# Kernel tuning notes

Hardware: AMD Instinct MI355X
Metric: run time of the kernel (lower is better)

The kernel has to match this reference:

```python
import jax, jax.numpy as jnp
import numpy as np

D_MODEL = 1024
N_HEADS = 16
D_K = D_MODEL // N_HEADS
SCALE = float(np.sqrt(D_K))


def setup_inputs() -> dict:
    key = jax.random.key(0)
    ks = jax.random.split(key, 6)
    B, S = 2, 2048
    lim_qkv = 1.0 / np.sqrt(D_MODEL)
    x = jax.random.normal(ks[0], (B, S, D_MODEL), dtype=jnp.float32)
    mask = jnp.ones((B, S), dtype=jnp.int32)
    W_qkv = jax.random.uniform(ks[1], (D_MODEL, 3 * D_MODEL), jnp.float32, -lim_qkv, lim_qkv)
    b_qkv = jax.random.uniform(ks[2], (3 * D_MODEL,), jnp.float32, -lim_qkv, lim_qkv)
    W_out = jax.random.uniform(ks[3], (D_MODEL, D_MODEL), jnp.float32, -lim_qkv, lim_qkv)
    b_out = jax.random.uniform(ks[4], (D_MODEL,), jnp.float32, -lim_qkv, lim_qkv)
    return {"x": x, "mask": mask, "W_qkv": W_qkv, "b_qkv": b_qkv, "W_out": W_out, "b_out": b_out}


def reference(x, mask, W_qkv, b_qkv, W_out, b_out):
    B, S, _ = x.shape
    qkv = x @ W_qkv + b_qkv                                  # [B,S,3*D]
    qkv = qkv.reshape(B, S, 3, N_HEADS, D_K)
    qkv = jnp.transpose(qkv, (2, 0, 3, 1, 4))                # [3,B,H,S,Dk]
    q, k, v = qkv[0], qkv[1], qkv[2]
    scores = jnp.einsum('bhqd,bhkd->bhqk', q, k) / SCALE      # [B,H,S,S]
    m = mask[:, None, None, :]                               # [B,1,1,S]
    scores = jnp.where(m == 0, jnp.float32(-1e9), scores)
    attn = jax.nn.softmax(scores, axis=-1)
    out = jnp.einsum('bhqk,bhkd->bhqd', attn, v)             # [B,H,S,Dk]
    out = jnp.transpose(out, (0, 2, 1, 3)).reshape(B, S, D_MODEL)
    return out @ W_out + b_out
```

## Files before the change

kernel.cpp:

```cpp
#include <hip/hip_runtime.h>
#include <hip/hip_bf16.h>

typedef __attribute__((ext_vector_type(8))) short short8;
typedef __attribute__((ext_vector_type(4))) short short4v;
typedef __attribute__((ext_vector_type(4))) float f32x4;
typedef __attribute__((ext_vector_type(16))) float f32x16;
typedef __attribute__((ext_vector_type(4))) unsigned uint4v;
typedef __attribute__((ext_vector_type(2))) unsigned uint2v;

static constexpr int BATCH = 2, S = 2048, D = 1024, H = 16, DK = 64;
static constexpr int TOK = BATCH * S;
static constexpr int NQKV = 3 * D;
static constexpr float C2 = 0.125f * 1.44269504088896f;

__device__ inline unsigned short f2bf(float f) {
  unsigned int u = __builtin_bit_cast(unsigned int, f);
  unsigned int r = (u + 0x7fffu + ((u >> 16) & 1u)) >> 16;
  return (unsigned short)r;
}

__device__ inline unsigned cvt_pk_bf16(float lo, float hi) {
  unsigned r;
  asm("v_cvt_pk_bf16_f32 %0, %1, %2" : "=v"(r) : "v"(lo), "v"(hi));
  return r;
}

__device__ inline uint2v permswap(unsigned a, unsigned b) {
  return __builtin_amdgcn_permlane32_swap(a, b, false, false);
}

__device__ inline float fexp2(float x) { return __builtin_amdgcn_exp2f(x); }

__device__ inline void gload_lds16(const void* g, void* l) {
  __builtin_amdgcn_global_load_lds((const __attribute__((address_space(1))) void*)g,
                                   (__attribute__((address_space(3))) void*)l, 16, 0, 0);
}

static constexpr int NB_CVT  = (TOK * D / 4) / 256;
static constexpr int NB_WQKV = (NQKV / 64) * (D / 64);
static constexpr int NB_WOUT = (D / 64) * (D / 64);
static constexpr int NB_MASK = TOK / 256;

__global__ __launch_bounds__(256) void k_prep(const float* __restrict__ x,
                                              unsigned short* __restrict__ x_bf,
                                              const float* __restrict__ W_qkv,
                                              unsigned short* __restrict__ wqkv_t,
                                              const float* __restrict__ W_out,
                                              unsigned short* __restrict__ wout_t,
                                              const int* __restrict__ mask,
                                              float* __restrict__ maskadd,
                                              unsigned char* __restrict__ tileflags) {
  __shared__ float tile[64][65];
  const int bi = blockIdx.x;
  const int tid = threadIdx.x;
  if (bi < NB_CVT) {
    const int i = bi * 256 + tid;
    const float4 v = ((const float4*)x)[i];
    short4v o;
    o[0] = (short)f2bf(v.x); o[1] = (short)f2bf(v.y);
    o[2] = (short)f2bf(v.z); o[3] = (short)f2bf(v.w);
    ((short4v*)x_bf)[i] = o;
    return;
  }
  if (bi < NB_CVT + NB_WQKV + NB_WOUT) {
    const int tbi = bi - NB_CVT;
    const float* in; unsigned short* out; int C, bx, by;
    if (tbi < NB_WQKV) { in = W_qkv; out = wqkv_t; C = NQKV; bx = tbi % (NQKV / 64); by = tbi / (NQKV / 64); }
    else { const int u = tbi - NB_WQKV; in = W_out; out = wout_t; C = D; bx = u % (D / 64); by = u / (D / 64); }
    const int bc = bx * 64, br = by * 64;
    const int lrow = tid >> 4, lc4 = (tid & 15) * 4;
#pragma unroll
    for (int p = 0; p < 4; ++p) {
      const float4 v = *(const float4*)(in + (size_t)(br + p * 16 + lrow) * C + bc + lc4);
      tile[p * 16 + lrow][lc4 + 0] = v.x;
      tile[p * 16 + lrow][lc4 + 1] = v.y;
      tile[p * 16 + lrow][lc4 + 2] = v.z;
      tile[p * 16 + lrow][lc4 + 3] = v.w;
    }
    __syncthreads();
    const int c = tid >> 2, seg = (tid & 3) * 16;
    uint4v w0, w1;
#pragma unroll
    for (int j = 0; j < 4; ++j) {
      w0[j] = cvt_pk_bf16(tile[seg + 2 * j][c], tile[seg + 2 * j + 1][c]);
      w1[j] = cvt_pk_bf16(tile[seg + 8 + 2 * j][c], tile[seg + 9 + 2 * j][c]);
    }
    unsigned short* dst = out + (size_t)(bc + c) * D + br + seg;
    *(uint4v*)dst = w0;
    *(uint4v*)(dst + 8) = w1;
    return;
  }
  {
    const int j = (bi - NB_CVT - NB_WQKV - NB_WOUT) * 256 + tid;
    const int mv = mask[j];
    maskadd[j] = mv ? 0.f : -1.0e9f;
    const unsigned long long bal = __ballot(mv == 0);
    if ((tid & 63) == 0) tileflags[j >> 6] = (bal != 0ull) ? 1 : 0;
  }
}

template <int QKV_MODE>
__global__ __launch_bounds__(256, 3) void k_gemm(const unsigned short* __restrict__ A,
                                                 const unsigned short* __restrict__ Bt,
                                                 const float* __restrict__ bias,
                                                 void* __restrict__ Cout,
                                                 unsigned short* __restrict__ vt,
                                                 int M, int N, int K) {
  __shared__ alignas(16) unsigned short As[128 * 64];
  __shared__ alignas(16) unsigned short Bs[128 * 64];
  const int tid = threadIdx.x;
  const int wid = tid >> 6, lane = tid & 63;
  const int lr = lane & 15, lg = lane >> 4;
  const int nbx = N >> 7;
  const int bx = blockIdx.x % nbx, by = blockIdx.x / nbx;
  const int m0 = by << 7, n0 = bx << 7;
  const int wm = (wid >> 1) << 6, wn = (wid & 1) << 6;

  f32x4 acc[4][4] = {};

  const int sk = ((lane & 7) ^ (lane >> 3)) << 4;
  const int srow = lane >> 3;

  const int ktc = K >> 6;
  for (int kt = 0; kt < ktc; ++kt) {
    const int k0 = kt << 6;
    __syncthreads();
#pragma unroll
    for (int c = 0; c < 4; ++c) {
      const int chunk = c * 4 + wid;
      const int mrow = chunk * 8 + srow;
      const char* ga = (const char*)(A + (size_t)(m0 + mrow) * K + k0) + sk;
      gload_lds16(ga, (char*)As + chunk * 1024);
      const char* gb = (const char*)(Bt + (size_t)(n0 + mrow) * K + k0) + sk;
      gload_lds16(gb, (char*)Bs + chunk * 1024);
    }
    __syncthreads();
#pragma unroll
    for (int ks = 0; ks < 2; ++ks) {
      const int kb = ks * 64 + lg * 16;
      const int swz = (lr & 7) << 4;
      short8 af[4], bfr[4];
#pragma unroll
      for (int mf = 0; mf < 4; ++mf) {
        const int m = wm + mf * 16 + lr;
        af[mf] = *(const short8*)((const char*)As + m * 128 + (kb ^ swz));
      }
#pragma unroll
      for (int nf = 0; nf < 4; ++nf) {
        const int n = wn + nf * 16 + lr;
        bfr[nf] = *(const short8*)((const char*)Bs + n * 128 + (kb ^ swz));
      }
#pragma unroll
      for (int mf = 0; mf < 4; ++mf)
#pragma unroll
        for (int nf = 0; nf < 4; ++nf)
          acc[mf][nf] = __builtin_amdgcn_mfma_f32_16x16x32_bf16(af[mf], bfr[nf], acc[mf][nf], 0, 0, 0);
    }
  }
#pragma unroll
  for (int nf = 0; nf < 4; ++nf) {
    const int n = n0 + wn + nf * 16 + lr;
    const float bv = bias[n];
    if (QKV_MODE) {
      if (n < 2 * D) {
        const float scl = (n < D) ? C2 : 1.0f;
#pragma unroll
        for (int mf = 0; mf < 4; ++mf)
#pragma unroll
          for (int r = 0; r < 4; ++r) {
            const int m = m0 + wm + mf * 16 + lg * 4 + r;
            ((unsigned short*)Cout)[(size_t)m * N + n] = f2bf((acc[mf][nf][r] + bv) * scl);
          }
      } else {
        const int dd = n - 2 * D;
        const int hh = dd >> 6, dk = dd & 63;
#pragma unroll
        for (int mf = 0; mf < 4; ++mf) {
          const int mbase = m0 + wm + mf * 16 + lg * 4;
          const int bb = mbase >> 11;
          const int ss = mbase & (S - 1);
          uint2 w;
          w.x = cvt_pk_bf16(acc[mf][nf][0] + bv, acc[mf][nf][1] + bv);
          w.y = cvt_pk_bf16(acc[mf][nf][2] + bv, acc[mf][nf][3] + bv);
          *(uint2*)(vt + ((size_t)((bb * H + hh) * DK + dk)) * S + ss) = w;
        }
      }
    } else {
#pragma unroll
      for (int mf = 0; mf < 4; ++mf)
#pragma unroll
        for (int r = 0; r < 4; ++r) {
          const int m = m0 + wm + mf * 16 + lg * 4 + r;
          ((float*)Cout)[(size_t)m * N + n] = acc[mf][nf][r] + bv;
        }
    }
  }
}

__global__ __launch_bounds__(256, 2) void k_attn(const unsigned short* __restrict__ qkv,
                                                 const unsigned short* __restrict__ vt,
                                                 const float* __restrict__ maskadd,
                                                 const unsigned char* __restrict__ tileflags,
                                                 unsigned short* __restrict__ attn) {
  __shared__ alignas(16) char Ks[2][16384];
  __shared__ alignas(16) char Vs[2][16384];

  constexpr int NT = S / 128;

  const int blk = blockIdx.x;
  const int work = (blk & 7) * 64 + (blk >> 3);
  const int qt = work & 15;
  const int bh = work >> 4;
  const int b = bh >> 4, h = bh & 15;
  const int tid = threadIdx.x;
  const int wid = tid >> 6, lane = tid & 63;
  const int l5 = lane & 31, hw = lane >> 5;
  const int q0 = qt * 128 + wid * 32;
  const int q = q0 + l5;

  const unsigned char* bflags = tileflags + b * (S / 64);

  const unsigned short* qrow = qkv + (size_t)(b * S + q) * NQKV + h * DK;
  short8 qf[4];
#pragma unroll
  for (int ks = 0; ks < 4; ++ks)
    qf[ks] = *(const short8*)(qrow + ks * 16 + hw * 8);

  const unsigned short* kg0 = qkv + ((size_t)b * S * NQKV + D + h * DK);
  const unsigned short* vg0 = vt + (size_t)bh * DK * S;
  const int srow8 = lane >> 3;
  const int skk = ((lane & 7) ^ srow8) << 4;
  const int vrow4 = lane >> 4;

  auto stage = [&](int buf, int kt) {
    const int kbase = kt * 128;
#pragma unroll
    for (int i = 0; i < 4; ++i) {
      const int ck = wid + i * 4;
      const int krow = ck * 8 + srow8;
      gload_lds16((const char*)(kg0 + (size_t)(kbase + krow) * NQKV) + skk,
                  Ks[buf] + ck * 1024);
      const int cv = wid + i * 4;
      const int vr = cv * 4 + vrow4;
      const int ss = (lane & 15) ^ (vr & 15);
      gload_lds16((const char*)(vg0 + (size_t)vr * S + kbase + ss * 8),
                  Vs[buf] + cv * 1024);
    }
  };

  f32x16 o[2] = {};
  float lpart = 0.f;

  const int rswz8 = (l5 & 7) << 4;
  const int rswz16 = (l5 & 15) << 4;

  stage(0, 0);

  int cur = 0;
  for (int kt = 0; kt < NT; ++kt) {
    asm volatile("s_waitcnt vmcnt(0)" ::: "memory");
    __builtin_amdgcn_s_barrier();
    __builtin_amdgcn_sched_barrier(0);
    if (kt + 1 < NT) stage(cur ^ 1, kt + 1);

    const int kbase = kt * 128;

    f32x16 sc[4];
    __builtin_amdgcn_s_setprio(1);
#pragma unroll
    for (int kh = 0; kh < 4; ++kh) {
      f32x16 t2 = {};
#pragma unroll
      for (int ks = 0; ks < 4; ++ks) {
        const short8 kf = *(const short8*)(Ks[cur] + (kh * 32 + l5) * 128 +
                                           ((ks * 32 + hw * 16) ^ rswz8));
        t2 = __builtin_amdgcn_mfma_f32_32x32x16_bf16(kf, qf[ks], t2, 0, 0, 0);
      }
      sc[kh] = t2;
    }
    __builtin_amdgcn_s_setprio(0);

    short8 vf[2][8];
#pragma unroll
    for (int dh = 0; dh < 2; ++dh)
#pragma unroll
      for (int s = 0; s < 8; ++s)
        vf[dh][s] = *(const short8*)(Vs[cur] + (dh * 32 + l5) * 256 +
                                     ((s * 32 + hw * 16) ^ rswz16));

    if (bflags[2 * kt] | bflags[2 * kt + 1]) {
#pragma unroll
      for (int kh = 0; kh < 4; ++kh)
#pragma unroll
        for (int m = 0; m < 4; ++m) {
          const f32x4 a4 = *(const f32x4*)(maskadd + b * S + kbase + kh * 32 + m * 8 + hw * 4);
#pragma unroll
          for (int r = 0; r < 4; ++r)
            sc[kh][m * 4 + r] += a4[r];
        }
    }

    float ps = 0.f;
#pragma unroll
    for (int kh = 0; kh < 4; ++kh) {
#pragma unroll
      for (int r = 0; r < 16; ++r)
        sc[kh][r] = fexp2(sc[kh][r]);
#pragma unroll
      for (int m = 0; m < 4; ++m)
        ps += (sc[kh][4 * m] + sc[kh][4 * m + 1]) + (sc[kh][4 * m + 2] + sc[kh][4 * m + 3]);

      const unsigned c00 = cvt_pk_bf16(sc[kh][0], sc[kh][1]);
      const unsigned c01 = cvt_pk_bf16(sc[kh][2], sc[kh][3]);
      const unsigned c10 = cvt_pk_bf16(sc[kh][4], sc[kh][5]);
      const unsigned c11 = cvt_pk_bf16(sc[kh][6], sc[kh][7]);
      const unsigned c20 = cvt_pk_bf16(sc[kh][8], sc[kh][9]);
      const unsigned c21 = cvt_pk_bf16(sc[kh][10], sc[kh][11]);
      const unsigned c30 = cvt_pk_bf16(sc[kh][12], sc[kh][13]);
      const unsigned c31 = cvt_pk_bf16(sc[kh][14], sc[kh][15]);
      const uint2v r0 = permswap(c00, c10);
      const uint2v r1 = permswap(c01, c11);
      const uint2v r2 = permswap(c20, c30);
      const uint2v r3 = permswap(c21, c31);
      uint4v p0, p1;
      p0[0] = r0[0]; p0[2] = r0[1]; p0[1] = r1[0]; p0[3] = r1[1];
      p1[0] = r2[0]; p1[2] = r2[1]; p1[1] = r3[0]; p1[3] = r3[1];
      const short8 pb0 = __builtin_bit_cast(short8, p0);
      const short8 pb1 = __builtin_bit_cast(short8, p1);

      __builtin_amdgcn_s_setprio(1);
#pragma unroll
      for (int dh = 0; dh < 2; ++dh) {
        o[dh] = __builtin_amdgcn_mfma_f32_32x32x16_bf16(vf[dh][2 * kh], pb0, o[dh], 0, 0, 0);
        o[dh] = __builtin_amdgcn_mfma_f32_32x32x16_bf16(vf[dh][2 * kh + 1], pb1, o[dh], 0, 0, 0);
      }
      __builtin_amdgcn_s_setprio(0);
    }
    lpart += ps;

    cur ^= 1;
  }

  const float ls = lpart + __shfl_xor(lpart, 32);
  const float inv = 1.0f / ls;
  unsigned short* orow = attn + (size_t)(b * S + q) * D + h * DK;
#pragma unroll
  for (int dh = 0; dh < 2; ++dh)
#pragma unroll
    for (int m = 0; m < 4; ++m) {
      const int d = dh * 32 + m * 8 + hw * 4;
      uint2 w;
      w.x = cvt_pk_bf16(o[dh][4 * m + 0] * inv, o[dh][4 * m + 1] * inv);
      w.y = cvt_pk_bf16(o[dh][4 * m + 2] * inv, o[dh][4 * m + 3] * inv);
      *(uint2*)(orow + d) = w;
    }
}

extern "C" void kernel_launch(void* const* d_in, const int* in_sizes, int n_in,
                              void* d_out, int out_size, void* d_ws, size_t ws_size,
                              hipStream_t stream) {
  const float* x = (const float*)d_in[0];
  const int* mask = (const int*)d_in[1];
  const float* W_qkv = (const float*)d_in[2];
  const float* b_qkv = (const float*)d_in[3];
  const float* W_out = (const float*)d_in[4];
  const float* b_out = (const float*)d_in[5];
  float* out = (float*)d_out;

  char* ws = (char*)d_ws;
  unsigned short* x_bf   = (unsigned short*)(ws);
  unsigned short* wqkv_t = (unsigned short*)(ws + (size_t)(8 << 20));
  unsigned short* wout_t = (unsigned short*)(ws + (size_t)(14 << 20));
  unsigned short* qkv    = (unsigned short*)(ws + (size_t)(16 << 20));
  unsigned short* vtr    = (unsigned short*)(ws + (size_t)(40 << 20));
  unsigned short* attn   = (unsigned short*)(ws + (size_t)(48 << 20));
  float*          madd   = (float*)(ws + (size_t)(56 << 20));
  unsigned char*  tflags = (unsigned char*)(ws + (size_t)(56 << 20) + 16384);

  k_prep<<<NB_CVT + NB_WQKV + NB_WOUT + NB_MASK, 256, 0, stream>>>(
      x, x_bf, W_qkv, wqkv_t, W_out, wout_t, mask, madd, tflags);
  k_gemm<1><<<(TOK / 128) * (NQKV / 128), 256, 0, stream>>>(x_bf, wqkv_t, b_qkv, qkv, vtr, TOK, NQKV, D);
  k_attn<<<BATCH * H * (S / 128), 256, 0, stream>>>(qkv, vtr, madd, tflags, attn);
  k_gemm<0><<<(TOK / 128) * (D / 128), 256, 0, stream>>>(attn, wout_t, b_out, out, nullptr, TOK, D, D);
}
```

Measured before the change: 107.1 us.

## Rewrite QKV GEMM as 256x256 tile, 8-wave, double-buffered LDS pipeline

Result: slower. 121.1 us (+13.0%).

```diff
diff --git a/kernel.cpp b/kernel.cpp
--- a/kernel.cpp
+++ b/kernel.cpp
@@ -99,13 +99,154 @@
   }
 }
 
-template <int QKV_MODE>
-__global__ __launch_bounds__(256, 3) void k_gemm(const unsigned short* __restrict__ A,
-                                                 const unsigned short* __restrict__ Bt,
-                                                 const float* __restrict__ bias,
-                                                 void* __restrict__ Cout,
-                                                 unsigned short* __restrict__ vt,
-                                                 int M, int N, int K) {
+__global__ __launch_bounds__(512, 1) void k_gemm_qkv(const unsigned short* __restrict__ A,
+                                                     const unsigned short* __restrict__ Bt,
+                                                     const float* __restrict__ bias,
+                                                     unsigned short* __restrict__ qkv,
+                                                     unsigned short* __restrict__ vt) {
+  constexpr int K = D;
+  constexpr int N = NQKV;
+  __shared__ alignas(16) char As[2][2][16384];
+  __shared__ alignas(16) char Bs[2][2][16384];
+
+  const int tid = threadIdx.x;
+  const int wid = tid >> 6, lane = tid & 63;
+  const int lr = lane & 15, lg = lane >> 4;
+  const int wave_m = wid >> 2, wave_n = wid & 3;
+
+  const int blk = blockIdx.x;
+  const int work = (blk & 7) * 24 + (blk >> 3);
+  const int bx = work % 12, by = work / 12;
+  const int m0 = by * 256, n0 = bx * 256;
+
+  const int srow = lane >> 3;
+  const int sk = ((lane & 7) ^ srow) << 4;
+
+  f32x4 acc[8][4] = {};
+
+  auto stageA = [&](int d, int h, int k) {
+#pragma unroll
+    for (int c = 0; c < 2; ++c) {
+      const int chunk = c * 8 + wid;
+      const int row = chunk * 8 + srow;
+      gload_lds16((const char*)(A + (size_t)(m0 + h * 128 + row) * K + k * 64) + sk,
+                  &As[d][h][chunk * 1024]);
+    }
+  };
+  auto stageB = [&](int d, int h, int k) {
+#pragma unroll
+    for (int c = 0; c < 2; ++c) {
+      const int chunk = c * 8 + wid;
+      const int row = chunk * 8 + srow;
+      gload_lds16((const char*)(Bt + (size_t)(n0 + h * 128 + row) * K + k * 64) + sk,
+                  &Bs[d][h][chunk * 1024]);
+    }
+  };
+
+  stageA(0, 0, 0); stageA(0, 1, 0); stageB(0, 0, 0); stageB(0, 1, 0);
+  stageA(1, 0, 1); stageA(1, 1, 1); stageB(1, 0, 1); stageB(1, 1, 1);
+  asm volatile("s_waitcnt vmcnt(8)" ::: "memory");
+  __builtin_amdgcn_s_barrier();
+  __builtin_amdgcn_sched_barrier(0);
+
+  const int rsw = (lr & 7) << 4;
+  const int nbase = (wave_n & 1) * 64;
+
+  for (int it = 0; it < 8; ++it) {
+    const int k1 = 2 * it + 1;
+    const int k2 = 2 * it + 2;
+#pragma unroll
+    for (int p = 0; p < 8; ++p) {
+      const int g = p >> 2;
+      const int mh = (p >> 1) & 1, nh = p & 1;
+      const char* Ab = &As[g][wave_m][0];
+      const char* Bb = &Bs[g][wave_n >> 1][0];
+
+      short8 af[4][2], bfr[2][2];
+#pragma unroll
+      for (int j = 0; j < 4; ++j) {
+        const int row = (mh * 4 + j) * 16 + lr;
+#pragma unroll
+        for (int ks = 0; ks < 2; ++ks)
+          af[j][ks] = *(const short8*)(Ab + row * 128 + ((ks * 64 + lg * 16) ^ rsw));
+      }
+#pragma unroll
+      for (int j2 = 0; j2 < 2; ++j2) {
+        const int row = nbase + (nh * 2 + j2) * 16 + lr;
+#pragma unroll
+        for (int ks = 0; ks < 2; ++ks)
+          bfr[j2][ks] = *(const short8*)(Bb + row * 128 + ((ks * 64 + lg * 16) ^ rsw));
+      }
+
+      if (g == 0) {
+        if (it > 0) {
+          if (p == 0) stageA(1, 0, k1);
+          else if (p == 1) stageA(1, 1, k1);
+          else if (p == 2) stageB(1, 0, k1);
+          else stageB(1, 1, k1);
+        }
+      } else {
+        if (it < 7) {
+          if (p == 4) stageA(0, 0, k2);
+          else if (p == 5) stageA(0, 1, k2);
+          else if (p == 6) stageB(0, 0, k2);
+          else stageB(0, 1, k2);
+        }
+      }
+      if (p == 3 || p == 7) asm volatile("s_waitcnt vmcnt(0)" ::: "memory");
+      __builtin_amdgcn_s_barrier();
+      __builtin_amdgcn_sched_barrier(0);
+
+      __builtin_amdgcn_s_setprio(1);
+#pragma unroll
+      for (int j = 0; j < 4; ++j)
+#pragma unroll
+        for (int j2 = 0; j2 < 2; ++j2)
+#pragma unroll
+          for (int ks = 0; ks < 2; ++ks)
+            acc[mh * 4 + j][nh * 2 + j2] = __builtin_amdgcn_mfma_f32_16x16x32_bf16(
+                af[j][ks], bfr[j2][ks], acc[mh * 4 + j][nh * 2 + j2], 0, 0, 0);
+      __builtin_amdgcn_s_setprio(0);
+      __builtin_amdgcn_s_barrier();
+      __builtin_amdgcn_sched_barrier(0);
+    }
+  }
+
+#pragma unroll
+  for (int nf = 0; nf < 4; ++nf) {
+    const int n = n0 + wave_n * 64 + nf * 16 + lr;
+    const float bv = bias[n];
+    if (n < 2 * D) {
+      const float scl = (n < D) ? C2 : 1.0f;
+#pragma unroll
+      for (int mf = 0; mf < 8; ++mf)
+#pragma unroll
+        for (int r = 0; r < 4; ++r) {
+          const int m = m0 + wave_m * 128 + mf * 16 + lg * 4 + r;
+          qkv[(size_t)m * N + n] = f2bf((acc[mf][nf][r] + bv) * scl);
+        }
+    } else {
+      const int dd = n - 2 * D;
+      const int hh = dd >> 6, dk = dd & 63;
+#pragma unroll
+      for (int mf = 0; mf < 8; ++mf) {
+        const int mbase = m0 + wave_m * 128 + mf * 16 + lg * 4;
+        const int bb = mbase >> 11;
+        const int ss = mbase & (S - 1);
+        uint2 w;
+        w.x = cvt_pk_bf16(acc[mf][nf][0] + bv, acc[mf][nf][1] + bv);
+        w.y = cvt_pk_bf16(acc[mf][nf][2] + bv, acc[mf][nf][3] + bv);
+        *(uint2*)(vt + ((size_t)((bb * H + hh) * DK + dk)) * S + ss) = w;
+      }
+    }
+  }
+}
+
+__global__ __launch_bounds__(256, 3) void k_gemm_out(const unsigned short* __restrict__ A,
+                                                     const unsigned short* __restrict__ Bt,
+                                                     const float* __restrict__ bias,
+                                                     float* __restrict__ Cout,
+                                                     int M, int N, int K) {
   __shared__ alignas(16) unsigned short As[128 * 64];
   __shared__ alignas(16) unsigned short Bs[128 * 64];
   const int tid = threadIdx.x;
@@ -161,39 +302,13 @@
   for (int nf = 0; nf < 4; ++nf) {
     const int n = n0 + wn + nf * 16 + lr;
     const float bv = bias[n];
-    if (QKV_MODE) {
-      if (n < 2 * D) {
-        const float scl = (n < D) ? C2 : 1.0f;
-#pragma unroll
-        for (int mf = 0; mf < 4; ++mf)
-#pragma unroll
-          for (int r = 0; r < 4; ++r) {
-            const int m = m0 + wm + mf * 16 + lg * 4 + r;
-            ((unsigned short*)Cout)[(size_t)m * N + n] = f2bf((acc[mf][nf][r] + bv) * scl);
-          }
-      } else {
-        const int dd = n - 2 * D;
-        const int hh = dd >> 6, dk = dd & 63;
-#pragma unroll
-        for (int mf = 0; mf < 4; ++mf) {
-          const int mbase = m0 + wm + mf * 16 + lg * 4;
-          const int bb = mbase >> 11;
-          const int ss = mbase & (S - 1);
-          uint2 w;
-          w.x = cvt_pk_bf16(acc[mf][nf][0] + bv, acc[mf][nf][1] + bv);
-          w.y = cvt_pk_bf16(acc[mf][nf][2] + bv, acc[mf][nf][3] + bv);
-          *(uint2*)(vt + ((size_t)((bb * H + hh) * DK + dk)) * S + ss) = w;
-        }
-      }
-    } else {
-#pragma unroll
-      for (int mf = 0; mf < 4; ++mf)
-#pragma unroll
-        for (int r = 0; r < 4; ++r) {
-          const int m = m0 + wm + mf * 16 + lg * 4 + r;
-          ((float*)Cout)[(size_t)m * N + n] = acc[mf][nf][r] + bv;
-        }
-    }
+#pragma unroll
+    for (int mf = 0; mf < 4; ++mf)
+#pragma unroll
+      for (int r = 0; r < 4; ++r) {
+        const int m = m0 + wm + mf * 16 + lg * 4 + r;
+        Cout[(size_t)m * N + n] = acc[mf][nf][r] + bv;
+      }
   }
 }
 
@@ -379,7 +494,7 @@
 
   k_prep<<<NB_CVT + NB_WQKV + NB_WOUT + NB_MASK, 256, 0, stream>>>(
       x, x_bf, W_qkv, wqkv_t, W_out, wout_t, mask, madd, tflags);
-  k_gemm<1><<<(TOK / 128) * (NQKV / 128), 256, 0, stream>>>(x_bf, wqkv_t, b_qkv, qkv, vtr, TOK, NQKV, D);
+  k_gemm_qkv<<<(TOK / 256) * (NQKV / 256), 512, 0, stream>>>(x_bf, wqkv_t, b_qkv, qkv, vtr);
   k_attn<<<BATCH * H * (S / 128), 256, 0, stream>>>(qkv, vtr, madd, tflags, attn);
-  k_gemm<0><<<(TOK / 128) * (D / 128), 256, 0, stream>>>(attn, wout_t, b_out, out, nullptr, TOK, D, D);
-}
+  k_gemm_out<<<(TOK / 128) * (D / 128), 256, 0, stream>>>(attn, wout_t, b_out, out, TOK, D, D);
+}
```
